# Performance work log

Measured on AMD Instinct MI355X. Metric: run time of the kernel, lower is better.

Reference implementation:

```python
import jax, jax.numpy as jnp
import numpy as np
import math

B, S, D, H, R = 4, 2048, 512, 8, 8  # R = k+1 relative slots per direction


def setup_inputs() -> dict:
    key = jax.random.key(0)
    ks = jax.random.split(key, 16)
    dk = D // H
    sc = 1.0 / math.sqrt(D)
    return {
        "query": jax.random.normal(ks[0], (B, S, D), jnp.float32),
        "key": jax.random.normal(ks[1], (B, S, D), jnp.float32),
        "value": jax.random.normal(ks[2], (B, S, D), jnp.float32),
        "start_nodes": jax.random.randint(ks[3], (B, H, R, S), 0, S, jnp.int64 if jax.config.jax_enable_x64 else jnp.int32),
        "end_nodes": jax.random.randint(ks[4], (B, H, R, S), 0, S, jnp.int64 if jax.config.jax_enable_x64 else jnp.int32),
        "rel_q": jax.random.normal(ks[5], (1, H, 2 * R, dk), jnp.float32),
        "rel_k": jax.random.normal(ks[6], (1, H, 2 * R, dk), jnp.float32),
        "rel_v": jax.random.normal(ks[7], (1, H, 2 * R, dk), jnp.float32),
        "Wq": jax.random.normal(ks[8], (D, D), jnp.float32) * sc,
        "bq": jnp.zeros((D,), jnp.float32),
        "Wk": jax.random.normal(ks[9], (D, D), jnp.float32) * sc,
        "bk": jnp.zeros((D,), jnp.float32),
        "Wv": jax.random.normal(ks[10], (D, D), jnp.float32) * sc,
        "bv": jnp.zeros((D,), jnp.float32),
        "Wo": jax.random.normal(ks[11], (D, D), jnp.float32) * sc,
        "bo": jnp.zeros((D,), jnp.float32),
    }


def reference(query, key, value, start_nodes, end_nodes, rel_q, rel_k, rel_v,
              Wq, bq, Wk, bk, Wv, bv, Wo, bo):
    Bs, Ss, Ds = query.shape
    Hs = start_nodes.shape[1]
    dk = Ds // Hs

    def proj(x, W, b):
        return (x @ W.T + b).reshape(Bs, Ss, Hs, dk).transpose(0, 2, 1, 3)  # [B,H,S,dk]

    q = proj(query, Wq, bq)
    k = proj(key, Wk, bk)
    v = proj(value, Wv, bv)

    start_mask = start_nodes == -1
    sn = jnp.where(start_mask, 0, start_nodes)  # -1 padding -> 0 (masked out below)
    qidx = jnp.concatenate([end_nodes, sn], axis=2)  # [B,H,2R,S]
    kidx = jnp.concatenate([sn, end_nodes], axis=2)

    bi = jnp.arange(Bs)[:, None, None, None]
    hi = jnp.arange(Hs)[None, :, None, None]
    q_ctx = q[bi, hi, qidx]  # [B,H,2R,S,dk]
    k_ctx = k[bi, hi, kidx]
    v_ctx = v[bi, hi, kidx]

    # c2c + c2p + p2c, scale_factor = 3 (rel_q and rel_k both provided)
    scores = ((q_ctx * k_ctx).sum(-1)
              + (q_ctx * rel_k[:, :, :, None, :]).sum(-1)
              + (rel_q[:, :, :, None, :] * k_ctx).sum(-1))
    scores = scores / (3.0 * jnp.sqrt(jnp.asarray(dk, scores.dtype)))

    # mask: padded edges masked in both halves; first S flat entries always masked
    mask = jnp.concatenate([start_mask, start_mask], axis=2).reshape(Bs, Hs, -1)
    mask = mask.at[:, :, :Ss].set(True)
    sflat = jnp.exp(jnp.where(mask, -1e9, scores.reshape(Bs, Hs, -1)))  # [B,H,2R*S]

    qf = qidx.reshape(Bs, Hs, -1)
    b2 = jnp.arange(Bs)[:, None, None]
    h2 = jnp.arange(Hs)[None, :, None]
    # scatter-add softmax denominator over destination nodes, then gather back
    denom = jnp.zeros((Bs, Hs, Ss), sflat.dtype).at[b2, h2, qf].add(sflat)
    denom = jnp.where(denom == 0, -1e9, denom)
    probs = (sflat / denom[b2, h2, qf]).reshape(Bs, Hs, -1, Ss, 1)  # [B,H,2R,S,1]

    attn_v = probs * (v_ctx + rel_v[:, :, :, None, :])  # [B,H,2R,S,dk]
    out = jnp.zeros((Bs, Hs, Ss, dk), attn_v.dtype).at[b2, h2, qf].add(
        attn_v.reshape(Bs, Hs, -1, dk))  # scatter-add aggregation over edges

    out = out.transpose(0, 2, 1, 3).reshape(Bs, Ss, Ds)
    return out @ Wo.T + bo
```

## Files before the change

kernel.cpp:

```cpp
#include <hip/hip_runtime.h>
#include <math.h>

#define B_ 4
#define S_ 2048
#define D_ 512
#define H_ 8
#define R_ 8
#define DK_ 64
#define EPB   (2*R_*S_)
#define ELLCAP 64

typedef __attribute__((ext_vector_type(8))) short bf16x8;
typedef __attribute__((ext_vector_type(8))) unsigned short ushort8_t;
typedef __attribute__((ext_vector_type(4))) float f32x4;

#define AS1q const __attribute__((address_space(1)))
#define AS3q __attribute__((address_space(3)))

__device__ inline unsigned short f2bf(float f) {
    unsigned u = __builtin_bit_cast(unsigned, f);
    u += 0x7fffu + ((u >> 16) & 1u);
    return (unsigned short)(u >> 16);
}
__device__ inline float bf2f(unsigned short u) {
    return __builtin_bit_cast(float, ((unsigned)u) << 16);
}

__global__ __launch_bounds__(256) void prep(
    const float* __restrict__ query, const float* __restrict__ key,
    const float* __restrict__ value,
    const float* __restrict__ Wq, const float* __restrict__ Wk,
    const float* __restrict__ Wv, const float* __restrict__ Wo,
    const float* __restrict__ rel_q, const float* __restrict__ rel_k,
    const float* __restrict__ rel_v,
    unsigned short* __restrict__ qc, unsigned short* __restrict__ kc_,
    unsigned short* __restrict__ vc,
    unsigned short* __restrict__ wqp, unsigned short* __restrict__ wkp,
    unsigned short* __restrict__ wvp, unsigned short* __restrict__ wop,
    unsigned short* __restrict__ rqb, unsigned short* __restrict__ rkb,
    unsigned short* __restrict__ rvb)
{
    int bid = blockIdx.x;
    int t = threadIdx.x;
    if (bid < 12288) {
        int z = bid >> 12;
        const float* x = (z == 0) ? query : (z == 1) ? key : value;
        unsigned short* y = (z == 0) ? qc : (z == 1) ? kc_ : vc;
        size_t i = ((size_t)(bid & 4095) * 256 + t) * 4;
        float4 v = *(const float4*)&x[i];
        *(ushort4*)&y[i] = make_ushort4(f2bf(v.x), f2bf(v.y), f2bf(v.z), f2bf(v.w));
    } else if (bid < 12800) {
        int r = bid - 12288;
        int z = r >> 7;
        const float* x = (z == 0) ? Wq : (z == 1) ? Wk : (z == 2) ? Wv : Wo;
        unsigned short* y = (z == 0) ? wqp : (z == 1) ? wkp : (z == 2) ? wvp : wop;
        int fi = (r & 127) * 256 + t;
        int ng   = fi >> 10;
        int kc   = (fi >> 6) & 15;
        int lane = fi & 63;
        const float* src = x + (size_t)(ng * 16 + (lane & 15)) * D_
                             + kc * 32 + (lane >> 4) * 8;
        float4 a0 = *(const float4*)src;
        float4 a1 = *(const float4*)(src + 4);
        ushort8_t c;
        c[0] = f2bf(a0.x); c[1] = f2bf(a0.y); c[2] = f2bf(a0.z); c[3] = f2bf(a0.w);
        c[4] = f2bf(a1.x); c[5] = f2bf(a1.y); c[6] = f2bf(a1.z); c[7] = f2bf(a1.w);
        *(ushort8_t*)&y[(size_t)fi * 8] = c;
    } else {
        int rr = bid - 12800;
        int z = rr >> 3;
        const float* x = (z == 0) ? rel_q : (z == 1) ? rel_k : rel_v;
        unsigned short* y = (z == 0) ? rqb : (z == 1) ? rkb : rvb;
        size_t i = ((size_t)(rr & 7) * 256 + t) * 4;
        float4 v = *(const float4*)&x[i];
        *(ushort4*)&y[i] = make_ushort4(f2bf(v.x), f2bf(v.y), f2bf(v.z), f2bf(v.w));
    }
}

__global__ __launch_bounds__(256) void gemm_qkv(
    const unsigned short* __restrict__ A0, const unsigned short* __restrict__ A1,
    const unsigned short* __restrict__ A2,
    const unsigned short* __restrict__ W0, const unsigned short* __restrict__ W1,
    const unsigned short* __restrict__ W2,
    const float* __restrict__ bi0, const float* __restrict__ bi1, const float* __restrict__ bi2,
    unsigned short* __restrict__ C0, unsigned short* __restrict__ C1,
    unsigned short* __restrict__ C2)
{
    __shared__ unsigned short As[128 * 64];
    const int bi  = blockIdx.x;
    const int xcd = bi & 7;
    const int r   = bi >> 3;
    const int z   = r >> 5;
    const int rr  = r & 31;
    const int m0  = (xcd * 8 + (rr >> 2)) * 128;
    const int n0  = (rr & 3) * 128;

    const unsigned short* A = (z == 0) ? A0 : (z == 1) ? A1 : A2;
    const unsigned short* W = (z == 0) ? W0 : (z == 1) ? W1 : W2;
    const float* bias       = (z == 0) ? bi0 : (z == 1) ? bi1 : bi2;
    unsigned short* C       = (z == 0) ? C0 : (z == 1) ? C1 : C2;

    const int t    = threadIdx.x;
    const int lane = t & 63;
    const int w    = t >> 6;
    const int wm   = w >> 1, wn = w & 1;
    const int lr    = lane >> 3;
    const int cglob = (lane & 7) ^ lr;

    f32x4 acc[4][4] = {};

    for (int kk = 0; kk < D_; kk += 64) {
        #pragma unroll
        for (int i = 0; i < 4; ++i) {
            int rowl = w * 32 + i * 8;
            const unsigned short* ga =
                A + (size_t)(m0 + rowl + lr) * D_ + kk + cglob * 8;
            __builtin_amdgcn_global_load_lds((AS1q unsigned*)ga,
                (AS3q unsigned*)(As + rowl * 64), 16, 0, 0);
        }
        __syncthreads();

        #pragma unroll
        for (int ks = 0; ks < 64; ks += 32) {
            const int c0 = ks >> 3;
            const int kc = (kk + ks) >> 5;
            bf16x8 af[4], bfr[4];
            #pragma unroll
            for (int mi = 0; mi < 4; ++mi) {
                int row = wm * 64 + mi * 16 + (lane & 15);
                int cp  = (c0 + (lane >> 4)) ^ (lane & 7);
                af[mi] = *(const bf16x8*)&As[row * 64 + cp * 8];
            }
            #pragma unroll
            for (int nj = 0; nj < 4; ++nj) {
                int ng = (n0 >> 4) + wn * 4 + nj;
                bfr[nj] = *(const bf16x8*)&W[(size_t)((ng * 16 + kc) << 6) * 8 + lane * 8];
            }
            #pragma unroll
            for (int mi = 0; mi < 4; ++mi)
                #pragma unroll
                for (int nj = 0; nj < 4; ++nj)
                    acc[mi][nj] = __builtin_amdgcn_mfma_f32_16x16x32_bf16(af[mi], bfr[nj], acc[mi][nj], 0, 0, 0);
        }
        __syncthreads();
    }

    #pragma unroll
    for (int mi = 0; mi < 4; ++mi) {
        #pragma unroll
        for (int nj = 0; nj < 4; ++nj) {
            #pragma unroll
            for (int rg = 0; rg < 4; ++rg) {
                int m = m0 + wm * 64 + mi * 16 + (lane >> 4) * 4 + rg;
                int n = n0 + wn * 64 + nj * 16 + (lane & 15);
                float val = acc[mi][nj][rg] + bias[n];
                int b = m >> 11, s = m & (S_ - 1);
                int h = n >> 6,  d = n & 63;
                C[((((size_t)b * H_ + h) * S_ + s) << 6) + d] = f2bf(val);
            }
        }
    }
}

__global__ __launch_bounds__(256) void gemm_out(
    const unsigned short* __restrict__ A, const unsigned short* __restrict__ W,
    const float* __restrict__ bias, float* __restrict__ Cf)
{
    __shared__ unsigned short As[128 * 64];
    const int bi  = blockIdx.x;
    const int xcd = bi & 7;
    const int r   = bi >> 3;
    const int m0  = (xcd * 8 + (r >> 3)) * 128;
    const int n0  = (r & 7) * 64;

    const int t    = threadIdx.x;
    const int lane = t & 63;
    const int w    = t >> 6;
    const int wm   = w >> 1, wn = w & 1;
    const int lr    = lane >> 3;
    const int cglob = (lane & 7) ^ lr;

    f32x4 acc[4][2] = {};

    for (int kk = 0; kk < D_; kk += 64) {
        #pragma unroll
        for (int i = 0; i < 4; ++i) {
            int rowl = w * 32 + i * 8;
            int m = m0 + rowl + lr;
            int b = m >> 11, s = m & (S_ - 1), h = kk >> 6;
            const unsigned short* ga =
                A + ((((size_t)b * H_ + h) * S_ + s) << 6) + cglob * 8;
            __builtin_amdgcn_global_load_lds((AS1q unsigned*)ga,
                (AS3q unsigned*)(As + rowl * 64), 16, 0, 0);
        }
        __syncthreads();

        #pragma unroll
        for (int ks = 0; ks < 64; ks += 32) {
            const int c0 = ks >> 3;
            const int kc = (kk + ks) >> 5;
            bf16x8 af[4], bfr[2];
            #pragma unroll
            for (int mi = 0; mi < 4; ++mi) {
                int row = wm * 64 + mi * 16 + (lane & 15);
                int cp  = (c0 + (lane >> 4)) ^ (lane & 7);
                af[mi] = *(const bf16x8*)&As[row * 64 + cp * 8];
            }
            #pragma unroll
            for (int nj = 0; nj < 2; ++nj) {
                int ng = (n0 >> 4) + wn * 2 + nj;
                bfr[nj] = *(const bf16x8*)&W[(size_t)((ng * 16 + kc) << 6) * 8 + lane * 8];
            }
            #pragma unroll
            for (int mi = 0; mi < 4; ++mi)
                #pragma unroll
                for (int nj = 0; nj < 2; ++nj)
                    acc[mi][nj] = __builtin_amdgcn_mfma_f32_16x16x32_bf16(af[mi], bfr[nj], acc[mi][nj], 0, 0, 0);
        }
        __syncthreads();
    }

    #pragma unroll
    for (int mi = 0; mi < 4; ++mi) {
        #pragma unroll
        for (int nj = 0; nj < 2; ++nj) {
            #pragma unroll
            for (int rg = 0; rg < 4; ++rg) {
                int m = m0 + wm * 64 + mi * 16 + (lane >> 4) * 4 + rg;
                int n = n0 + wn * 32 + nj * 16 + (lane & 15);
                Cf[(size_t)m * D_ + n] = acc[mi][nj][rg] + bias[n];
            }
        }
    }
}

__global__ __launch_bounds__(1024) void attn_fused(
    const unsigned short* __restrict__ q, const unsigned short* __restrict__ k_,
    const unsigned short* __restrict__ v_,
    const unsigned short* __restrict__ rel_q, const unsigned short* __restrict__ rel_k,
    const unsigned short* __restrict__ rel_v,
    const int* __restrict__ start_nodes, const int* __restrict__ end_nodes,
    unsigned short* __restrict__ attn)
{
    __shared__ unsigned short ell[128 * ELLCAP];
    __shared__ int cnt[128];
    const int bi  = blockIdx.x;
    const int xcd = bi & 7;
    const int loc = bi >> 3;
    const int bh  = xcd * 4 + (loc >> 4);
    const int dlo = (loc & 15) << 7;
    const int t   = threadIdx.x;

    if (t < 128) cnt[t] = 0;
    __syncthreads();

    const int base_idx = bh * (R_ * S_);
    for (int f = t; f < EPB; f += 1024) {
        int r2 = f >> 11;
        if (r2 == 0) continue;
        int s = f & (S_ - 1);
        int idx = base_idx + (r2 & 7) * S_ + s;
        int sn = start_nodes[idx];
        if (sn == -1) continue;
        int en = end_nodes[idx];
        int dst = (r2 < R_) ? en : sn;
        unsigned rel = (unsigned)(dst - dlo);
        if (rel < 128u) {
            int ki = (r2 < R_) ? sn : en;
            int pos = atomicAdd(&cnt[rel], 1);
            if (pos < ELLCAP)
                ell[(rel << 6) + pos] = (unsigned short)((r2 << 11) | ki);
        }
    }
    __syncthreads();

    const int w    = t >> 6;
    const int lane = t & 63;
    const int grp  = lane >> 3;
    const int sub  = lane & 7;
    const int h    = bh & 7;
    const size_t node_base = ((size_t)bh << 11);

    for (int dd = 0; dd < 8; ++dd) {
        int dl  = dd * 16 + w;
        int dst = dlo + dl;

        ushort8_t q8 = *(const ushort8_t*)&q[((node_base + dst) << 6) + sub * 8];
        float qv[8];
        #pragma unroll
        for (int i = 0; i < 8; ++i) qv[i] = bf2f(q8[i]);

        int n = cnt[dl];
        if (n > ELLCAP) n = ELLCAP;
        int d_all = (int)ell[(dl << 6) + lane];

        float den = 0.f;
        float o[8] = {};
        #pragma unroll 2
        for (int j = 0; j < n; j += 8) {
            int slot = j + grp;
            int d = __shfl(d_all, slot);
            bool valid = slot < n;
            int ki = d & (S_ - 1);
            int r2 = (d >> 11) & 15;
            ushort8_t k8  = *(const ushort8_t*)&k_  [((node_base + ki) << 6) + sub * 8];
            ushort8_t rk8 = *(const ushort8_t*)&rel_k[(((h << 4) + r2) << 6) + sub * 8];
            ushort8_t rq8 = *(const ushort8_t*)&rel_q[(((h << 4) + r2) << 6) + sub * 8];
            float p = 0.f;
            #pragma unroll
            for (int i = 0; i < 8; ++i)
                p = fmaf(bf2f(k8[i]), qv[i] + bf2f(rq8[i]),
                         fmaf(qv[i], bf2f(rk8[i]), p));
            p += __shfl_xor(p, 1);
            p += __shfl_xor(p, 2);
            p += __shfl_xor(p, 4);
            float sf = valid ? __expf(p * (1.0f / 24.0f)) : 0.f;
            ushort8_t v8  = *(const ushort8_t*)&v_  [((node_base + ki) << 6) + sub * 8];
            ushort8_t rv8 = *(const ushort8_t*)&rel_v[(((h << 4) + r2) << 6) + sub * 8];
            den += sf;
            #pragma unroll
            for (int i = 0; i < 8; ++i)
                o[i] = fmaf(sf, bf2f(v8[i]) + bf2f(rv8[i]), o[i]);
        }
        den += __shfl_xor(den, 8); den += __shfl_xor(den, 16); den += __shfl_xor(den, 32);
        #pragma unroll
        for (int i = 0; i < 8; ++i) {
            o[i] += __shfl_xor(o[i], 8);
            o[i] += __shfl_xor(o[i], 16);
            o[i] += __shfl_xor(o[i], 32);
        }
        if (grp == 0) {
            float inv = (den > 0.f) ? 1.0f / den : 0.f;
            ushort8_t rs;
            #pragma unroll
            for (int i = 0; i < 8; ++i) rs[i] = f2bf(o[i] * inv);
            *(ushort8_t*)&attn[((node_base + dst) << 6) + sub * 8] = rs;
        }
    }
}

extern "C" void kernel_launch(void* const* d_in, const int* in_sizes, int n_in,
                              void* d_out, int out_size, void* d_ws, size_t ws_size,
                              hipStream_t stream) {
    const float* query = (const float*)d_in[0];
    const float* key   = (const float*)d_in[1];
    const float* value = (const float*)d_in[2];
    const int* start_nodes = (const int*)d_in[3];
    const int* end_nodes   = (const int*)d_in[4];
    const float* rel_q = (const float*)d_in[5];
    const float* rel_k = (const float*)d_in[6];
    const float* rel_v = (const float*)d_in[7];
    const float* Wq = (const float*)d_in[8];
    const float* bq = (const float*)d_in[9];
    const float* Wk = (const float*)d_in[10];
    const float* bk = (const float*)d_in[11];
    const float* Wv = (const float*)d_in[12];
    const float* bv = (const float*)d_in[13];
    const float* Wo = (const float*)d_in[14];
    const float* bo = (const float*)d_in[15];
    float* out = (float*)d_out;

    const size_t NQ = (size_t)B_ * H_ * S_ * DK_;
    const size_t NW = (size_t)D_ * D_;
    const size_t NR = (size_t)H_ * 2 * R_ * DK_;
    unsigned short* p = (unsigned short*)d_ws;
    unsigned short* qc = p;            p += NQ;
    unsigned short* kc = p;            p += NQ;
    unsigned short* vc = p;            p += NQ;
    unsigned short* q  = p;            p += NQ;
    unsigned short* k  = p;            p += NQ;
    unsigned short* v  = p;            p += NQ;
    unsigned short* attn = p;          p += NQ;
    unsigned short* wqp = p;           p += NW;
    unsigned short* wkp = p;           p += NW;
    unsigned short* wvp = p;           p += NW;
    unsigned short* wop = p;           p += NW;
    unsigned short* rqb = p;           p += NR;
    unsigned short* rkb = p;           p += NR;
    unsigned short* rvb = p;           p += NR;

    prep<<<12824, 256, 0, stream>>>(query, key, value, Wq, Wk, Wv, Wo,
                                    rel_q, rel_k, rel_v,
                                    qc, kc, vc, wqp, wkp, wvp, wop,
                                    rqb, rkb, rvb);

    gemm_qkv<<<768, 256, 0, stream>>>(qc, kc, vc, wqp, wkp, wvp,
                                      bq, bk, bv, q, k, v);

    attn_fused<<<512, 1024, 0, stream>>>(q, k, v, rqb, rkb, rvb,
                                         start_nodes, end_nodes, attn);

    gemm_out<<<512, 256, 0, stream>>>(attn, wop, bo, out);
}
```

Baseline: 223.5 us.

## Pre-pack activations into MFMA fragment layout and drop LDS staging in GEMMs

The prep kernel now writes the query/key/value bf16 copies directly in the per-lane MFMA fragment order already used for the weights. The attention kernel likewise writes its output in that packed layout. Both GEMMs then load A fragments straight from global memory with one 16-byte load per lane, removing the LDS tile, the global_load_lds staging and the barriers. This gives up LDS reuse of A tiles across waves sharing rows, so A traffic now depends on L1/L2 hits, and there is no software prefetch beyond an unroll of 2.

```diff
diff --git a/kernel.cpp b/kernel.cpp
--- a/kernel.cpp
+++ b/kernel.cpp
@@ -14,9 +14,6 @@
 typedef __attribute__((ext_vector_type(8))) unsigned short ushort8_t;
 typedef __attribute__((ext_vector_type(4))) float f32x4;
 
-#define AS1q const __attribute__((address_space(1)))
-#define AS3q __attribute__((address_space(3)))
-
 __device__ inline unsigned short f2bf(float f) {
     unsigned u = __builtin_bit_cast(unsigned, f);
     u += 0x7fffu + ((u >> 16) & 1u);
@@ -33,8 +30,8 @@
     const float* __restrict__ Wv, const float* __restrict__ Wo,
     const float* __restrict__ rel_q, const float* __restrict__ rel_k,
     const float* __restrict__ rel_v,
-    unsigned short* __restrict__ qc, unsigned short* __restrict__ kc_,
-    unsigned short* __restrict__ vc,
+    unsigned short* __restrict__ aq, unsigned short* __restrict__ ak,
+    unsigned short* __restrict__ av,
     unsigned short* __restrict__ wqp, unsigned short* __restrict__ wkp,
     unsigned short* __restrict__ wvp, unsigned short* __restrict__ wop,
     unsigned short* __restrict__ rqb, unsigned short* __restrict__ rkb,
@@ -42,24 +39,28 @@
 {
     int bid = blockIdx.x;
     int t = threadIdx.x;
-    if (bid < 12288) {
-        int z = bid >> 12;
-        const float* x = (z == 0) ? query : (z == 1) ? key : value;
-        unsigned short* y = (z == 0) ? qc : (z == 1) ? kc_ : vc;
-        size_t i = ((size_t)(bid & 4095) * 256 + t) * 4;
-        float4 v = *(const float4*)&x[i];
-        *(ushort4*)&y[i] = make_ushort4(f2bf(v.x), f2bf(v.y), f2bf(v.z), f2bf(v.w));
-    } else if (bid < 12800) {
-        int r = bid - 12288;
-        int z = r >> 7;
-        const float* x = (z == 0) ? Wq : (z == 1) ? Wk : (z == 2) ? Wv : Wo;
-        unsigned short* y = (z == 0) ? wqp : (z == 1) ? wkp : (z == 2) ? wvp : wop;
-        int fi = (r & 127) * 256 + t;
-        int ng   = fi >> 10;
+    if (bid < 6656) {
+        const float* x;
+        unsigned short* y;
+        int fi;
+        if (bid < 6144) {
+            int z = bid >> 11;
+            x = (z == 0) ? query : (z == 1) ? key : value;
+            y = (z == 0) ? aq : (z == 1) ? ak : av;
+            fi = (bid & 2047) * 256 + t;
+        } else {
+            int r = bid - 6144;
+            int z = r >> 7;
+            x = (z == 0) ? Wq : (z == 1) ? Wk : (z == 2) ? Wv : Wo;
+            y = (z == 0) ? wqp : (z == 1) ? wkp : (z == 2) ? wvp : wop;
+            fi = (r & 127) * 256 + t;
+        }
+        int lane = fi & 63;
+        int mg   = fi >> 10;
         int kc   = (fi >> 6) & 15;
-        int lane = fi & 63;
-        const float* src = x + (size_t)(ng * 16 + (lane & 15)) * D_
-                             + kc * 32 + (lane >> 4) * 8;
+        int row  = mg * 16 + (lane & 15);
+        int col  = kc * 32 + ((lane >> 4) << 3);
+        const float* src = x + (size_t)row * D_ + col;
         float4 a0 = *(const float4*)src;
         float4 a1 = *(const float4*)(src + 4);
         ushort8_t c;
@@ -67,7 +68,7 @@
         c[4] = f2bf(a1.x); c[5] = f2bf(a1.y); c[6] = f2bf(a1.z); c[7] = f2bf(a1.w);
         *(ushort8_t*)&y[(size_t)fi * 8] = c;
     } else {
-        int rr = bid - 12800;
+        int rr = bid - 6656;
         int z = rr >> 3;
         const float* x = (z == 0) ? rel_q : (z == 1) ? rel_k : rel_v;
         unsigned short* y = (z == 0) ? rqb : (z == 1) ? rkb : rvb;
@@ -86,14 +87,13 @@
     unsigned short* __restrict__ C0, unsigned short* __restrict__ C1,
     unsigned short* __restrict__ C2)
 {
-    __shared__ unsigned short As[128 * 64];
     const int bi  = blockIdx.x;
     const int xcd = bi & 7;
     const int r   = bi >> 3;
     const int z   = r >> 5;
     const int rr  = r & 31;
-    const int m0  = (xcd * 8 + (rr >> 2)) * 128;
-    const int n0  = (rr & 3) * 128;
+    const int mg0 = (xcd * 8 + (rr >> 2)) * 8;
+    const int ng0 = (rr & 3) * 8;
 
     const unsigned short* A = (z == 0) ? A0 : (z == 1) ? A1 : A2;
     const unsigned short* W = (z == 0) ? W0 : (z == 1) ? W1 : W2;
@@ -104,56 +104,38 @@
     const int lane = t & 63;
     const int w    = t >> 6;
     const int wm   = w >> 1, wn = w & 1;
-    const int lr    = lane >> 3;
-    const int cglob = (lane & 7) ^ lr;
 
     f32x4 acc[4][4] = {};
 
-    for (int kk = 0; kk < D_; kk += 64) {
-        #pragma unroll
-        for (int i = 0; i < 4; ++i) {
-            int rowl = w * 32 + i * 8;
-            const unsigned short* ga =
-                A + (size_t)(m0 + rowl + lr) * D_ + kk + cglob * 8;
-            __builtin_amdgcn_global_load_lds((AS1q unsigned*)ga,
-                (AS3q unsigned*)(As + rowl * 64), 16, 0, 0);
-        }
-        __syncthreads();
-
-        #pragma unroll
-        for (int ks = 0; ks < 64; ks += 32) {
-            const int c0 = ks >> 3;
-            const int kc = (kk + ks) >> 5;
-            bf16x8 af[4], bfr[4];
-            #pragma unroll
-            for (int mi = 0; mi < 4; ++mi) {
-                int row = wm * 64 + mi * 16 + (lane & 15);
-                int cp  = (c0 + (lane >> 4)) ^ (lane & 7);
-                af[mi] = *(const bf16x8*)&As[row * 64 + cp * 8];
-            }
-            #pragma unroll
-            for (int nj = 0; nj < 4; ++nj) {
-                int ng = (n0 >> 4) + wn * 4 + nj;
-                bfr[nj] = *(const bf16x8*)&W[(size_t)((ng * 16 + kc) << 6) * 8 + lane * 8];
-            }
-            #pragma unroll
-            for (int mi = 0; mi < 4; ++mi)
-                #pragma unroll
-                for (int nj = 0; nj < 4; ++nj)
-                    acc[mi][nj] = __builtin_amdgcn_mfma_f32_16x16x32_bf16(af[mi], bfr[nj], acc[mi][nj], 0, 0, 0);
-        }
-        __syncthreads();
+    #pragma unroll 2
+    for (int kc = 0; kc < 16; ++kc) {
+        bf16x8 af[4], bfr[4];
+        #pragma unroll
+        for (int fm = 0; fm < 4; ++fm) {
+            int mg = mg0 + wm * 4 + fm;
+            af[fm] = *(const bf16x8*)&A[(size_t)(((mg * 16 + kc) << 6) + lane) * 8];
+        }
+        #pragma unroll
+        for (int fn = 0; fn < 4; ++fn) {
+            int ng = ng0 + wn * 4 + fn;
+            bfr[fn] = *(const bf16x8*)&W[(size_t)(((ng * 16 + kc) << 6) + lane) * 8];
+        }
+        #pragma unroll
+        for (int fm = 0; fm < 4; ++fm)
+            #pragma unroll
+            for (int fn = 0; fn < 4; ++fn)
+                acc[fm][fn] = __builtin_amdgcn_mfma_f32_16x16x32_bf16(af[fm], bfr[fn], acc[fm][fn], 0, 0, 0);
     }
 
     #pragma unroll
-    for (int mi = 0; mi < 4; ++mi) {
-        #pragma unroll
-        for (int nj = 0; nj < 4; ++nj) {
+    for (int fm = 0; fm < 4; ++fm) {
+        #pragma unroll
+        for (int fn = 0; fn < 4; ++fn) {
             #pragma unroll
             for (int rg = 0; rg < 4; ++rg) {
-                int m = m0 + wm * 64 + mi * 16 + (lane >> 4) * 4 + rg;
-                int n = n0 + wn * 64 + nj * 16 + (lane & 15);
-                float val = acc[mi][nj][rg] + bias[n];
+                int m = (mg0 + wm * 4 + fm) * 16 + (lane >> 4) * 4 + rg;
+                int n = (ng0 + wn * 4 + fn) * 16 + (lane & 15);
+                float val = acc[fm][fn][rg] + bias[n];
                 int b = m >> 11, s = m & (S_ - 1);
                 int h = n >> 6,  d = n & 63;
                 C[((((size_t)b * H_ + h) * S_ + s) << 6) + d] = f2bf(val);
@@ -166,69 +148,48 @@
     const unsigned short* __restrict__ A, const unsigned short* __restrict__ W,
     const float* __restrict__ bias, float* __restrict__ Cf)
 {
-    __shared__ unsigned short As[128 * 64];
     const int bi  = blockIdx.x;
     const int xcd = bi & 7;
     const int r   = bi >> 3;
-    const int m0  = (xcd * 8 + (r >> 3)) * 128;
-    const int n0  = (r & 7) * 64;
+    const int mg0 = (xcd * 8 + (r >> 3)) * 8;
+    const int ng0 = (r & 7) * 4;
 
     const int t    = threadIdx.x;
     const int lane = t & 63;
     const int w    = t >> 6;
     const int wm   = w >> 1, wn = w & 1;
-    const int lr    = lane >> 3;
-    const int cglob = (lane & 7) ^ lr;
 
     f32x4 acc[4][2] = {};
 
-    for (int kk = 0; kk < D_; kk += 64) {
-        #pragma unroll
-        for (int i = 0; i < 4; ++i) {
-            int rowl = w * 32 + i * 8;
-            int m = m0 + rowl + lr;
-            int b = m >> 11, s = m & (S_ - 1), h = kk >> 6;
-            const unsigned short* ga =
-                A + ((((size_t)b * H_ + h) * S_ + s) << 6) + cglob * 8;
-            __builtin_amdgcn_global_load_lds((AS1q unsigned*)ga,
-                (AS3q unsigned*)(As + rowl * 64), 16, 0, 0);
-        }
-        __syncthreads();
-
-        #pragma unroll
-        for (int ks = 0; ks < 64; ks += 32) {
-            const int c0 = ks >> 3;
-            const int kc = (kk + ks) >> 5;
-            bf16x8 af[4], bfr[2];
-            #pragma unroll
-            for (int mi = 0; mi < 4; ++mi) {
-                int row = wm * 64 + mi * 16 + (lane & 15);
-                int cp  = (c0 + (lane >> 4)) ^ (lane & 7);
-                af[mi] = *(const bf16x8*)&As[row * 64 + cp * 8];
-            }
-            #pragma unroll
-            for (int nj = 0; nj < 2; ++nj) {
-                int ng = (n0 >> 4) + wn * 2 + nj;
-                bfr[nj] = *(const bf16x8*)&W[(size_t)((ng * 16 + kc) << 6) * 8 + lane * 8];
-            }
-            #pragma unroll
-            for (int mi = 0; mi < 4; ++mi)
-                #pragma unroll
-                for (int nj = 0; nj < 2; ++nj)
-                    acc[mi][nj] = __builtin_amdgcn_mfma_f32_16x16x32_bf16(af[mi], bfr[nj], acc[mi][nj], 0, 0, 0);
-        }
-        __syncthreads();
+    #pragma unroll 2
+    for (int kc = 0; kc < 16; ++kc) {
+        bf16x8 af[4], bfr[2];
+        #pragma unroll
+        for (int fm = 0; fm < 4; ++fm) {
+            int mg = mg0 + wm * 4 + fm;
+            af[fm] = *(const bf16x8*)&A[(size_t)(((mg * 16 + kc) << 6) + lane) * 8];
+        }
+        #pragma unroll
+        for (int fn = 0; fn < 2; ++fn) {
+            int ng = ng0 + wn * 2 + fn;
+            bfr[fn] = *(const bf16x8*)&W[(size_t)(((ng * 16 + kc) << 6) + lane) * 8];
+        }
+        #pragma unroll
+        for (int fm = 0; fm < 4; ++fm)
+            #pragma unroll
+            for (int fn = 0; fn < 2; ++fn)
+                acc[fm][fn] = __builtin_amdgcn_mfma_f32_16x16x32_bf16(af[fm], bfr[fn], acc[fm][fn], 0, 0, 0);
     }
 
     #pragma unroll
-    for (int mi = 0; mi < 4; ++mi) {
-        #pragma unroll
-        for (int nj = 0; nj < 2; ++nj) {
+    for (int fm = 0; fm < 4; ++fm) {
+        #pragma unroll
+        for (int fn = 0; fn < 2; ++fn) {
             #pragma unroll
             for (int rg = 0; rg < 4; ++rg) {
-                int m = m0 + wm * 64 + mi * 16 + (lane >> 4) * 4 + rg;
-                int n = n0 + wn * 32 + nj * 16 + (lane & 15);
-                Cf[(size_t)m * D_ + n] = acc[mi][nj][rg] + bias[n];
+                int m = (mg0 + wm * 4 + fm) * 16 + (lane >> 4) * 4 + rg;
+                int n = (ng0 + wn * 2 + fn) * 16 + (lane & 15);
+                Cf[(size_t)m * D_ + n] = acc[fm][fn][rg] + bias[n];
             }
         }
     }
@@ -334,7 +295,10 @@
             ushort8_t rs;
             #pragma unroll
             for (int i = 0; i < 8; ++i) rs[i] = f2bf(o[i] * inv);
-            *(ushort8_t*)&attn[((node_base + dst) << 6) + sub * 8] = rs;
+            int m  = ((bh >> 3) << 11) + dst;
+            int kc = (h << 1) + (sub >> 2);
+            int ln = (m & 15) + ((sub & 3) << 4);
+            *(ushort8_t*)&attn[(size_t)((((m >> 4) * 16 + kc) << 6) + ln) * 8] = rs;
         }
     }
 }
@@ -364,9 +328,9 @@
     const size_t NW = (size_t)D_ * D_;
     const size_t NR = (size_t)H_ * 2 * R_ * DK_;
     unsigned short* p = (unsigned short*)d_ws;
-    unsigned short* qc = p;            p += NQ;
-    unsigned short* kc = p;            p += NQ;
-    unsigned short* vc = p;            p += NQ;
+    unsigned short* aq = p;            p += NQ;
+    unsigned short* ak = p;            p += NQ;
+    unsigned short* av = p;            p += NQ;
     unsigned short* q  = p;            p += NQ;
     unsigned short* k  = p;            p += NQ;
     unsigned short* v  = p;            p += NQ;
@@ -379,12 +343,12 @@
     unsigned short* rkb = p;           p += NR;
     unsigned short* rvb = p;           p += NR;
 
-    prep<<<12824, 256, 0, stream>>>(query, key, value, Wq, Wk, Wv, Wo,
-                                    rel_q, rel_k, rel_v,
-                                    qc, kc, vc, wqp, wkp, wvp, wop,
-                                    rqb, rkb, rvb);
-
-    gemm_qkv<<<768, 256, 0, stream>>>(qc, kc, vc, wqp, wkp, wvp,
+    prep<<<6680, 256, 0, stream>>>(query, key, value, Wq, Wk, Wv, Wo,
+                                   rel_q, rel_k, rel_v,
+                                   aq, ak, av, wqp, wkp, wvp, wop,
+                                   rqb, rkb, rvb);
+
+    gemm_qkv<<<768, 256, 0, stream>>>(aq, ak, av, wqp, wkp, wvp,
                                       bq, bk, bv, q, k, v);
 
     attn_fused<<<512, 1024, 0, stream>>>(q, k, v, rqb, rkb, rvb,
```

Result: no change. 226.1 us (+1.2%).
